# Kernel tuning notes

Hardware: AMD Instinct MI355X
Metric: run time of the kernel (lower is better)

## Reference

```python
import jax, jax.numpy as jnp
import numpy as np

KERNEL = 3
SCALE = 2
PAD = KERNEL - 1
EPS = 1e-5


def _splits(a, s):
    # (B,C,W,H) -> (B,C,W/s,H/s,s*s), matching torch view/permute order
    B, C, W, H = a.shape
    b = a.reshape(B, C, s, W // s, s, H // s)
    b = jnp.transpose(b, (0, 1, 3, 5, 2, 4))
    return b.reshape(B, C, W // s, H // s, s * s)


def _p2o(psf, shape):
    # PSF (1,C,k,k) -> OTF (1,C,H,W)
    k_h, k_w = psf.shape[-2], psf.shape[-1]
    otf = jnp.zeros(psf.shape[:-2] + shape, dtype=psf.dtype)
    otf = otf.at[..., :k_h, :k_w].set(psf)
    otf = jnp.roll(otf, (-(k_h // 2), -(k_w // 2)), axis=(-2, -1))
    return jnp.fft.fftn(otf, axes=(-2, -1))


def _zero_upsample(x, s):
    B, C, H, W = x.shape
    z = jnp.zeros((B, C, H * s, W * s), dtype=x.dtype)
    return z.at[..., ::s, ::s].set(x)


def setup_inputs() -> dict:
    key = jax.random.key(0)
    kx, kw = jax.random.split(key)
    x = jax.random.normal(kx, (4, 64, 128, 128), dtype=jnp.float32)
    w = jax.random.normal(kw, (1, 64, KERNEL, KERNEL), dtype=jnp.float32)
    # init-time softmax over the k*k taps, as in the torch module
    w = jax.nn.softmax(w.reshape(1, 64, -1), axis=-1).reshape(1, 64, KERNEL, KERNEL)
    bias = jnp.zeros((1, 64, 1, 1), dtype=jnp.float32)
    return {"x": x, "weight": w, "bias": bias}


def reference(x, weight, bias):
    s = SCALE
    if PAD > 0:
        x = jnp.pad(x, ((0, 0), (0, 0), (PAD, PAD), (PAD, PAD)), mode="wrap")
    biaseps = jax.nn.sigmoid(bias - 9.0) + EPS  # (1,C,1,1)
    _, _, h, w = x.shape
    STy = _zero_upsample(x, s)
    # nearest-neighbor interpolate by integer scale == repeat
    x_up = jnp.repeat(jnp.repeat(x, s, axis=-2), s, axis=-1)
    FB = _p2o(weight, (h * s, w * s))          # (1,C,H,W) complex
    FBC = jnp.conj(FB)
    F2B = jnp.abs(FB) ** 2
    FBFy = FBC * jnp.fft.fftn(STy, axes=(-2, -1))
    FR = FBFy + jnp.fft.fftn(biaseps * x_up, axes=(-2, -1))
    x1 = FB * FR
    FBR = jnp.mean(_splits(x1, s), axis=-1)
    invW = jnp.mean(_splits(jnp.broadcast_to(F2B, x1.shape), s), axis=-1)
    invWBR = FBR / (invW + biaseps)
    FCBinvWBR = FBC * jnp.tile(invWBR, (1, 1, s, s))
    FX = (FR - FCBinvWBR) / biaseps
    out = jnp.real(jnp.fft.ifftn(FX, axes=(-2, -1)))
    if PAD > 0:
        c = PAD * s
        out = out[..., c:-c, c:-c]
    return jax.nn.gelu(out, approximate=False)
```

## Files before the change

kernel.cpp:

```cpp
#include <hip/hip_runtime.h>
#include <math.h>

#define NP   132
#define NV   67
#define NPP  (NP*NP)
#define NCH  64
#define NIMG 256
#define NX   128
#define NO   256
#define TWO_PI 6.2831853071795864769f

static const size_t OFF_H = 0;

#define TR0(t) (t.x)
#define TI0(t) (t.y)
#define TR1(t) (-(t.y))
#define TI1(t) (t.x)
#define TR2(t) (-(t.x))
#define TI2(t) (-(t.y))
#define TR3(t) (t.y)
#define TI3(t) (-(t.x))
#define CMACF(xr, xi, dr, di, TRv, TIv) { xr += (dr)*(TRv) + (di)*(TIv); xi += (di)*(TRv) - (dr)*(TIv); }
#define CMACG(xr, xi, dr, di, TRv, TIv) { xr += (dr)*(TRv) - (di)*(TIv); xi += (di)*(TRv) + (dr)*(TIv); }

__global__ __launch_bounds__(256) void k_compute_H(
    const float* __restrict__ wgt, const float* __restrict__ bias,
    float2* __restrict__ H) {
  int idx = blockIdx.x * 256 + threadIdx.x;
  int c = blockIdx.y;
  if (idx >= NV*NP) return;
  int u = idx % NP, v = idx / NP;
  float k[3][3];
#pragma unroll
  for (int i = 0; i < 3; i++)
#pragma unroll
    for (int j = 0; j < 3; j++) k[i][j] = wgt[c*9 + i*3 + j];
  float invW = 0.f;
#pragma unroll
  for (int p0 = -1; p0 <= 1; p0++)
#pragma unroll
    for (int p1 = -1; p1 <= 1; p1++) {
      float s = 0.f;
#pragma unroll
      for (int i = 0; i < 3; i++)
#pragma unroll
        for (int j = 0; j < 3; j++) {
          int i2 = i - 2*p0, j2 = j - 2*p1;
          if (i2 >= 0 && i2 < 3 && j2 >= 0 && j2 < 3) s += k[i][j]*k[i2][j2];
        }
      float ang = TWO_PI * (float)(u*p0 + v*p1) / (float)NP;
      invW += s * cosf(ang);
    }
  float B00 = k[0][0]+k[0][1]+k[1][0]+k[1][1];
  float B10 = k[2][0]+k[2][1];
  float B01 = k[0][2]+k[1][2];
  float B11 = k[2][2];
  float su, cu, sv, cv, suv, cuv;
  sincosf(TWO_PI*(float)u/(float)NP, &su, &cu);
  sincosf(TWO_PI*(float)v/(float)NP, &sv, &cv);
  sincosf(TWO_PI*(float)(u+v)/(float)NP, &suv, &cuv);
  float Bre = B00 + B10*cu + B01*cv + B11*cuv;
  float Bim = -(B10*su + B01*sv + B11*suv);
  float alpha = 1.f/(1.f + expf(9.f - bias[c])) + 1e-5f;
  float d = invW + alpha;
  H[((size_t)c*NV + v)*NP + u] = make_float2((1.f - Bre)/d, (-Bim)/d);
}

__global__ __launch_bounds__(1024, 4) void k_fused(
    const float* __restrict__ x, const float* __restrict__ wgt,
    const float2* __restrict__ H, float* __restrict__ out) {
  __shared__ __align__(16) float2 R1[67*134 + 4];
  __shared__ __align__(16) float2 R2[33*274];
  int tid = threadIdx.x;
  int img = blockIdx.x;
  int c = img & 63;
  const float* xim = x + (size_t)img*NX*NX;
  const float2* Hc = H + (size_t)c*NV*NP;
  float4* yb = (float4*)R1;

  for (int e = tid; e < 132*33; e += 1024) {
    int n1 = e % 132, rpg = e / 132;
    int col = (n1 + 126) & 127;
    int r0 = 4*rpg + 126;
    yb[n1*33 + rpg] = make_float4(
        xim[((r0    )&127)*NX + col],
        xim[((r0 + 1)&127)*NX + col],
        xim[((r0 + 2)&127)*NX + col],
        xim[((r0 + 3)&127)*NX + col]);
  }
  __syncthreads();

  {
    bool act = tid < 561;
    int rpg = 0, qq = 0;
    if (act) { rpg = tid/17; qq = tid - rpg*17; }
    int q2 = qq + 17;
    bool ph2 = (q2 >= 33);
    float sa_, ca_, sb_, cb_;
    sincosf(TWO_PI*(float)qq/33.f, &sa_, &ca_);
    sincosf(TWO_PI*(float)q2/33.f, &sb_, &cb_);
    float Sr[4][2][2], Si[4][2][2];
#pragma unroll
    for (int r = 0; r < 4; ++r)
#pragma unroll
      for (int g = 0; g < 2; ++g)
#pragma unroll
        for (int w = 0; w < 2; ++w) { Sr[r][g][w] = 0.f; Si[r][g][w] = 0.f; }
    if (act) {
      const float4* bp = yb + rpg;
      float tar = 1.f, tai = 0.f, tbr = 1.f, tbi = 0.f;
#pragma unroll 1
      for (int m = 0; m < 33; ++m) {
        float4 d0 = bp[0], d1 = bp[33], d2 = bp[66], d3 = bp[99];
#define S1M(r, dd) \
        CMACF(Sr[r][0][0], Si[r][0][0], dd.x, dd.y, tar, tai); \
        CMACF(Sr[r][0][1], Si[r][0][1], dd.z, dd.w, tar, tai); \
        CMACF(Sr[r][1][0], Si[r][1][0], dd.x, dd.y, tbr, tbi); \
        CMACF(Sr[r][1][1], Si[r][1][1], dd.z, dd.w, tbr, tbi);
        S1M(0, d0) S1M(1, d1) S1M(2, d2) S1M(3, d3)
#undef S1M
        { float nt = tar*ca_ - tai*sa_; tai = tar*sa_ + tai*ca_; tar = nt; }
        { float nt = tbr*cb_ - tbi*sb_; tbi = tbr*sb_ + tbi*cb_; tbr = nt; }
        bp += 132;
      }
    }
    __syncthreads();
    if (act) {
#pragma unroll
      for (int g = 0; g < 2; ++g) {
        if (g == 1 && ph2) continue;
        int q = g ? q2 : qq;
        float sw, cw; sincosf(TWO_PI*(float)q/132.f, &sw, &cw);
        float2 w1 = make_float2(cw, sw);
        float2 w2 = make_float2(cw*cw - sw*sw, 2.f*cw*sw);
        float2 w3 = make_float2(w2.x*cw - w2.y*sw, w2.x*sw + w2.y*cw);
#define S1C(sidx, P1, P2, P3) { \
        float z0r = Sr[0][g][0], z0i = Si[0][g][0], z1r = Sr[0][g][1], z1i = Si[0][g][1]; \
        CMACF(z0r, z0i, Sr[1][g][0], Si[1][g][0], TR##P1(w1), TI##P1(w1)); \
        CMACF(z1r, z1i, Sr[1][g][1], Si[1][g][1], TR##P1(w1), TI##P1(w1)); \
        CMACF(z0r, z0i, Sr[2][g][0], Si[2][g][0], TR##P2(w2), TI##P2(w2)); \
        CMACF(z1r, z1i, Sr[2][g][1], Si[2][g][1], TR##P2(w2), TI##P2(w2)); \
        CMACF(z0r, z0i, Sr[3][g][0], Si[3][g][0], TR##P3(w3), TI##P3(w3)); \
        CMACF(z1r, z1i, Sr[3][g][1], Si[3][g][1], TR##P3(w3), TI##P3(w3)); \
        yb[(q + 33*(sidx))*33 + rpg] = make_float4(z0r, z0i, z1r, z1i); }
        S1C(0,0,0,0) S1C(1,1,2,3) S1C(2,2,0,2) S1C(3,3,2,1)
#undef S1C
      }
    }
    __syncthreads();
    if (act) {
#pragma unroll
      for (int g = 0; g < 2; ++g) {
        if (g == 1 && ph2) continue;
        int q = g ? q2 : qq;
        float4 Za = yb[q*33 + rpg];
        float4 Zb = yb[((132 - q) % 132)*33 + rpg];
        float4 Zc = yb[(q + 33)*33 + rpg];
        float4 Zd = yb[(99 - q)*33 + rpg];
        float4* A4 = (float4*)&R2[rpg*274 + q*4];
        A4[0] = make_float4(0.5f*(Za.x+Zb.x), 0.5f*(Za.y-Zb.y),
                            0.5f*(Za.y+Zb.y), 0.5f*(Zb.x-Za.x));
        A4[1] = make_float4(0.5f*(Za.z+Zb.z), 0.5f*(Za.w-Zb.w),
                            0.5f*(Za.w+Zb.w), 0.5f*(Zb.z-Za.z));
        float4* B4 = (float4*)&R2[rpg*274 + (q+33)*4];
        B4[0] = make_float4(0.5f*(Zc.x+Zd.x), 0.5f*(Zc.y-Zd.y),
                            0.5f*(Zc.y+Zd.y), 0.5f*(Zd.x-Zc.x));
        B4[1] = make_float4(0.5f*(Zc.z+Zd.z), 0.5f*(Zc.w-Zd.w),
                            0.5f*(Zc.w+Zd.w), 0.5f*(Zd.z-Zc.z));
        if (q == 0) {
          float4 Ze = yb[66*33 + rpg];
          float4* C4 = (float4*)&R2[rpg*274 + 66*4];
          C4[0] = make_float4(Ze.x, 0.f, Ze.y, 0.f);
          C4[1] = make_float4(Ze.z, 0.f, Ze.w, 0.f);
        }
      }
    }
  }
  __syncthreads();

  {
    bool act = tid < 737;
    int v = 0, qq = 0;
    if (act) { v = tid/11; qq = tid - v*11; }
    float s11, c11; sincosf(TWO_PI*(float)qq/11.f, &s11, &c11);
    float s33q, c33q; sincosf(TWO_PI*(float)qq/33.f, &s33q, &c33q);
    const float CG = -0.5f, SG = 0.86602540378443864676f;
    float c33g[3], s33g[3];
    c33g[0] = c33q;               s33g[0] = s33q;
    c33g[1] = c33q*CG - s33q*SG;  s33g[1] = s33q*CG + c33q*SG;
    c33g[2] = c33q*CG + s33q*SG;  s33g[2] = s33q*CG - c33q*SG;
    float SSr[3][4], SSi[3][4];
    float Sr[4][3], Si[4][3];
    float2 h[3][4];
#define ZSS() { \
    _Pragma("unroll") for (int s = 0; s < 3; ++s) \
    _Pragma("unroll") for (int r = 0; r < 4; ++r) { SSr[s][r] = 0.f; SSi[s][r] = 0.f; } }
#define S23TLOOP(MAC) { \
    float tr = 1.f, ti = 0.f; \
    const float2* bp = R2 + v*4; \
    _Pragma("unroll 1") \
    for (int t = 0; t < 11; ++t) { \
      _Pragma("unroll") \
      for (int s = 0; s < 3; ++s) { \
        float4 d01 = *(const float4*)(bp + s*274); \
        float4 d23 = *(const float4*)(bp + s*274 + 2); \
        MAC(SSr[s][0], SSi[s][0], d01.x, d01.y, tr, ti); \
        MAC(SSr[s][1], SSi[s][1], d01.z, d01.w, tr, ti); \
        MAC(SSr[s][2], SSi[s][2], d23.x, d23.y, tr, ti); \
        MAC(SSr[s][3], SSi[s][3], d23.z, d23.w, tr, ti); } \
      { float nt = tr*c11 - ti*s11; ti = tr*s11 + ti*c11; tr = nt; } \
      bp += 3*274; \
    } }
#define S23COMB(MAC) { \
    _Pragma("unroll") \
    for (int g = 0; g < 3; ++g) { \
      float cA = c33g[g], sA = s33g[g]; \
      float cB = cA*cA - sA*sA, sB = 2.f*cA*sA; \
      _Pragma("unroll") \
      for (int r = 0; r < 4; ++r) { \
        float xr = SSr[0][r], xi = SSi[0][r]; \
        MAC(xr, xi, SSr[1][r], SSi[1][r], cA, sA); \
        MAC(xr, xi, SSr[2][r], SSi[2][r], cB, sB); \
        Sr[r][g] = xr; Si[r][g] = xi; } } }
    ZSS();
    if (act) {
      S23TLOOP(CMACF);
      S23COMB(CMACF);
#pragma unroll
      for (int g = 0; g < 3; ++g)
#pragma unroll
        for (int s = 0; s < 4; ++s)
          h[g][s] = Hc[(size_t)v*NP + (qq + 11*g) + 33*s];
    }
    __syncthreads();
    if (act) {
#pragma unroll
      for (int g = 0; g < 3; ++g) {
        int q = qq + 11*g;
        float sw, cw; sincosf(TWO_PI*(float)q/132.f, &sw, &cw);
        float2 w1 = make_float2(cw, sw);
        float2 w2 = make_float2(cw*cw - sw*sw, 2.f*cw*sw);
        float2 w3 = make_float2(w2.x*cw - w2.y*sw, w2.x*sw + w2.y*cw);
#define S23A(sidx, P1, P2, P3) { \
        int u = q + 33*(sidx); \
        float xr = Sr[0][g], xi = Si[0][g]; \
        CMACF(xr, xi, Sr[1][g], Si[1][g], TR##P1(w1), TI##P1(w1)); \
        CMACF(xr, xi, Sr[2][g], Si[2][g], TR##P2(w2), TI##P2(w2)); \
        CMACF(xr, xi, Sr[3][g], Si[3][g], TR##P3(w3), TI##P3(w3)); \
        float2 hh = h[g][sidx]; \
        R2[(u>>2)*274 + v*4 + (u&3)] = make_float2(xr*hh.x - xi*hh.y, xr*hh.y + xi*hh.x); }
        S23A(0,0,0,0) S23A(1,1,2,3) S23A(2,2,0,2) S23A(3,3,2,1)
#undef S23A
      }
    }
    __syncthreads();
    ZSS();
    if (act) {
      S23TLOOP(CMACG);
      S23COMB(CMACG);
#pragma unroll
      for (int g = 0; g < 3; ++g) {
        int q = qq + 11*g;
        float sw, cw; sincosf(TWO_PI*(float)q/132.f, &sw, &cw);
        float2 w1 = make_float2(cw, sw);
        float2 w2 = make_float2(cw*cw - sw*sw, 2.f*cw*sw);
        float2 w3 = make_float2(w2.x*cw - w2.y*sw, w2.x*sw + w2.y*cw);
#define S23B(sidx, P1, P2, P3) { \
        int n0 = q + 33*(sidx); \
        float xr = Sr[0][g], xi = Si[0][g]; \
        CMACG(xr, xi, Sr[1][g], Si[1][g], TR##P1(w1), TI##P1(w1)); \
        CMACG(xr, xi, Sr[2][g], Si[2][g], TR##P2(w2), TI##P2(w2)); \
        CMACG(xr, xi, Sr[3][g], Si[3][g], TR##P3(w3), TI##P3(w3)); \
        R1[v*134 + n0] = make_float2(xr, xi); }
        S23B(0,0,0,0) S23B(1,1,2,3) S23B(2,2,0,2) S23B(3,3,2,1)
#undef S23B
      }
    }
#undef S23TLOOP
#undef S23COMB
#undef ZSS
  }
  __syncthreads();

  {
    bool act = tid < 726;
    int j = 0, qq = 0;
    if (act) { j = tid/11; qq = tid - j*11; }
    float s11, c11; sincosf(TWO_PI*(float)qq/11.f, &s11, &c11);
    float s33q, c33q; sincosf(TWO_PI*(float)qq/33.f, &s33q, &c33q);
    const float CG = -0.5f, SG = 0.86602540378443864676f;
    float c33g[3], s33g[3];
    c33g[0] = c33q;               s33g[0] = s33q;
    c33g[1] = c33q*CG - s33q*SG;  s33g[1] = s33q*CG + c33q*SG;
    c33g[2] = c33q*CG + s33q*SG;  s33g[2] = s33q*CG - c33q*SG;
    float SSr[3][4], SSi[3][4];
#pragma unroll
    for (int s = 0; s < 3; ++s)
#pragma unroll
      for (int r = 0; r < 4; ++r) { SSr[s][r] = 0.f; SSi[s][r] = 0.f; }
    if (act) {
      const float2* Up = R1 + 2*j;
      float tr = 1.f, ti = 0.f;
#pragma unroll 1
      for (int t = 0; t < 11; ++t) {
#pragma unroll
        for (int s = 0; s < 3; ++s)
#pragma unroll
          for (int r = 0; r < 4; ++r) {
            int v4 = 12*t + 4*s + r;
            int vv = (v4 <= 66) ? v4 : (132 - v4);
            float sg = (v4 <= 66) ? 1.f : -1.f;
            float4 f = *(const float4*)(Up + vv*134);
            float Wr = f.x - sg*f.w;
            float Wi = sg*f.y + f.z;
            CMACG(SSr[s][r], SSi[s][r], Wr, Wi, tr, ti);
          }
        { float nt = tr*c11 - ti*s11; ti = tr*s11 + ti*c11; tr = nt; }
      }
      float Sr[4][3], Si[4][3];
#pragma unroll
      for (int g = 0; g < 3; ++g) {
        float cA = c33g[g], sA = s33g[g];
        float cB = cA*cA - sA*sA, sB = 2.f*cA*sA;
#pragma unroll
        for (int r = 0; r < 4; ++r) {
          float xr = SSr[0][r], xi = SSi[0][r];
          CMACG(xr, xi, SSr[1][r], SSi[1][r], cA, sA);
          CMACG(xr, xi, SSr[2][r], SSi[2][r], cB, sB);
          Sr[r][g] = xr; Si[r][g] = xi;
        }
      }
      float* rho2 = (float*)R2;
      const float scale = 1.0f/(float)NPP;
#pragma unroll
      for (int g = 0; g < 3; ++g) {
        int q = qq + 11*g;
        float sw, cw; sincosf(TWO_PI*(float)q/132.f, &sw, &cw);
        float2 w1 = make_float2(cw, sw);
        float2 w2 = make_float2(cw*cw - sw*sw, 2.f*cw*sw);
        float2 w3 = make_float2(w2.x*cw - w2.y*sw, w2.x*sw + w2.y*cw);
#define S4C(sidx, P1, P2, P3) { \
        int n1 = q + 33*(sidx); \
        float zr = Sr[0][g], zi = Si[0][g]; \
        CMACG(zr, zi, Sr[1][g], Si[1][g], TR##P1(w1), TI##P1(w1)); \
        CMACG(zr, zi, Sr[2][g], Si[2][g], TR##P2(w2), TI##P2(w2)); \
        CMACG(zr, zi, Sr[3][g], Si[3][g], TR##P3(w3), TI##P3(w3)); \
        rho2[(2*j)*136 + n1] = zr*scale; \
        rho2[(2*j+1)*136 + n1] = zi*scale; }
        S4C(0,0,0,0) S4C(1,1,2,3) S4C(2,2,0,2) S4C(3,3,2,1)
#undef S4C
      }
    }
  }
  __syncthreads();

  {
    const float* rho2 = (const float*)R2;
    const float* w = wgt + c*9;
    float k0=w[0], k1=w[1], k2=w[2], k3=w[3], k4=w[4], k5=w[5], k6=w[6], k7=w[7], k8=w[8];
    float* outim = out + (size_t)img*NO*NO;
    for (int e = tid; e < NO*NO; e += 1024) {
      int o1 = e & 255, o0 = e >> 8;
      int n0 = (o0 + 4) >> 1, n1 = (o1 + 4) >> 1;
      int p0 = o0 & 1, p1 = o1 & 1;
      int base = n0*136 + n1;
      float r00 = rho2[base],     r01 = rho2[base+1];
      float r10 = rho2[base+136], r11 = rho2[base+137];
      float wa = p0 ? (p1 ? k0 : k1) : (p1 ? k3 : k4);
      float wb = p1 ? (p0 ? k2 : k5) : 0.f;
      float wc = p0 ? (p1 ? k6 : k7) : 0.f;
      float wd = (p0 & p1) ? k8 : 0.f;
      float S = wa*r00 + wb*r01 + wc*r10 + wd*r11;
      float xv = xim[(n0-2)*NX + (n1-2)];
      float z = xv + S;
      outim[e] = 0.5f*z*(1.0f + erff(z*0.70710678118654752f));
    }
  }
}

extern "C" void kernel_launch(void* const* d_in, const int* in_sizes, int n_in,
                              void* d_out, int out_size, void* d_ws, size_t ws_size,
                              hipStream_t stream) {
  const float* x    = (const float*)d_in[0];
  const float* wgt  = (const float*)d_in[1];
  const float* bias = (const float*)d_in[2];
  float* ws = (float*)d_ws;
  float2* H = (float2*)(ws + OFF_H);
  float* out = (float*)d_out;

  k_compute_H<<<dim3((NV*NP + 255)/256, NCH), 256, 0, stream>>>(wgt, bias, H);
  k_fused<<<dim3(NIMG), 1024, 0, stream>>>(x, wgt, H, out);
}
```

Measured before the change: 155.4 us.

## Restructure first and last FFT stages to row-contiguous 3x4x11 decomposition with twiddle recurrences

New measurement: 144.0 us. -7.3%, faster.

```diff
diff --git a/kernel.cpp b/kernel.cpp
--- a/kernel.cpp
+++ b/kernel.cpp
@@ -76,73 +76,77 @@
   int c = img & 63;
   const float* xim = x + (size_t)img*NX*NX;
   const float2* Hc = H + (size_t)c*NV*NP;
-  float4* yb = (float4*)R1;
-
-  for (int e = tid; e < 132*33; e += 1024) {
-    int n1 = e % 132, rpg = e / 132;
+  const float CG = -0.5f,                  SG = 0.86602540378443864676f;
+  const float CR = 0.86602540378443864676f, SR = 0.5f;
+
+  float2* yb = R1;
+  for (int e = tid; e < 66*132; e += 1024) {
+    int n1 = e % 132, j = e / 132;
     int col = (n1 + 126) & 127;
-    int r0 = 4*rpg + 126;
-    yb[n1*33 + rpg] = make_float4(
-        xim[((r0    )&127)*NX + col],
-        xim[((r0 + 1)&127)*NX + col],
-        xim[((r0 + 2)&127)*NX + col],
-        xim[((r0 + 3)&127)*NX + col]);
+    int ra = (2*j + 126) & 127, rb = (2*j + 127) & 127;
+    yb[j*134 + n1] = make_float2(xim[ra*NX + col], xim[rb*NX + col]);
   }
   __syncthreads();
 
   {
-    bool act = tid < 561;
-    int rpg = 0, qq = 0;
-    if (act) { rpg = tid/17; qq = tid - rpg*17; }
-    int q2 = qq + 17;
-    bool ph2 = (q2 >= 33);
-    float sa_, ca_, sb_, cb_;
-    sincosf(TWO_PI*(float)qq/33.f, &sa_, &ca_);
-    sincosf(TWO_PI*(float)q2/33.f, &sb_, &cb_);
-    float Sr[4][2][2], Si[4][2][2];
-#pragma unroll
-    for (int r = 0; r < 4; ++r)
-#pragma unroll
-      for (int g = 0; g < 2; ++g)
-#pragma unroll
-        for (int w = 0; w < 2; ++w) { Sr[r][g][w] = 0.f; Si[r][g][w] = 0.f; }
-    if (act) {
-      const float4* bp = yb + rpg;
-      float tar = 1.f, tai = 0.f, tbr = 1.f, tbi = 0.f;
+    bool act = tid < 726;
+    int j = 0, qq = 0;
+    if (act) { j = tid/11; qq = tid - j*11; }
+    float s11, c11; sincosf(TWO_PI*(float)qq/11.f, &s11, &c11);
+    float s33q, c33q; sincosf(TWO_PI*(float)qq/33.f, &s33q, &c33q);
+    float swq, cwq; sincosf(TWO_PI*(float)qq/132.f, &swq, &cwq);
+    float c33g[3], s33g[3], cwg[3], swg[3];
+    c33g[0] = c33q; s33g[0] = s33q;
+    c33g[1] = c33q*CG - s33q*SG;       s33g[1] = s33q*CG + c33q*SG;
+    c33g[2] = c33g[1]*CG - s33g[1]*SG; s33g[2] = s33g[1]*CG + c33g[1]*SG;
+    cwg[0] = cwq; swg[0] = swq;
+    cwg[1] = cwq*CR - swq*SR;          swg[1] = swq*CR + cwq*SR;
+    cwg[2] = cwg[1]*CR - swg[1]*SR;    swg[2] = swg[1]*CR + cwg[1]*SR;
+    float SSr[3][4], SSi[3][4];
+#pragma unroll
+    for (int s = 0; s < 3; ++s)
+#pragma unroll
+      for (int r = 0; r < 4; ++r) { SSr[s][r] = 0.f; SSi[s][r] = 0.f; }
+    if (act) {
+      const float2* bp = yb + j*134;
+      float tr = 1.f, ti = 0.f;
 #pragma unroll 1
-      for (int m = 0; m < 33; ++m) {
-        float4 d0 = bp[0], d1 = bp[33], d2 = bp[66], d3 = bp[99];
-#define S1M(r, dd) \
-        CMACF(Sr[r][0][0], Si[r][0][0], dd.x, dd.y, tar, tai); \
-        CMACF(Sr[r][0][1], Si[r][0][1], dd.z, dd.w, tar, tai); \
-        CMACF(Sr[r][1][0], Si[r][1][0], dd.x, dd.y, tbr, tbi); \
-        CMACF(Sr[r][1][1], Si[r][1][1], dd.z, dd.w, tbr, tbi);
-        S1M(0, d0) S1M(1, d1) S1M(2, d2) S1M(3, d3)
-#undef S1M
-        { float nt = tar*ca_ - tai*sa_; tai = tar*sa_ + tai*ca_; tar = nt; }
-        { float nt = tbr*cb_ - tbi*sb_; tbi = tbr*sb_ + tbi*cb_; tbr = nt; }
-        bp += 132;
-      }
-    }
-    __syncthreads();
-    if (act) {
-#pragma unroll
-      for (int g = 0; g < 2; ++g) {
-        if (g == 1 && ph2) continue;
-        int q = g ? q2 : qq;
-        float sw, cw; sincosf(TWO_PI*(float)q/132.f, &sw, &cw);
-        float2 w1 = make_float2(cw, sw);
-        float2 w2 = make_float2(cw*cw - sw*sw, 2.f*cw*sw);
-        float2 w3 = make_float2(w2.x*cw - w2.y*sw, w2.x*sw + w2.y*cw);
+      for (int t = 0; t < 11; ++t) {
+#pragma unroll
+        for (int s = 0; s < 3; ++s) {
+          float4 d01 = *(const float4*)(bp + 12*t + 4*s);
+          float4 d23 = *(const float4*)(bp + 12*t + 4*s + 2);
+          CMACF(SSr[s][0], SSi[s][0], d01.x, d01.y, tr, ti);
+          CMACF(SSr[s][1], SSi[s][1], d01.z, d01.w, tr, ti);
+          CMACF(SSr[s][2], SSi[s][2], d23.x, d23.y, tr, ti);
+          CMACF(SSr[s][3], SSi[s][3], d23.z, d23.w, tr, ti);
+        }
+        { float nt = tr*c11 - ti*s11; ti = tr*s11 + ti*c11; tr = nt; }
+      }
+    }
+    float Zr[3][4], Zi[3][4];
+    if (act) {
+#pragma unroll
+      for (int g = 0; g < 3; ++g) {
+        float cA = c33g[g], sA = s33g[g];
+        float cB = cA*cA - sA*sA, sB = 2.f*cA*sA;
+        float Sr4[4], Si4[4];
+#pragma unroll
+        for (int r = 0; r < 4; ++r) {
+          float xr = SSr[0][r], xi = SSi[0][r];
+          CMACF(xr, xi, SSr[1][r], SSi[1][r], cA, sA);
+          CMACF(xr, xi, SSr[2][r], SSi[2][r], cB, sB);
+          Sr4[r] = xr; Si4[r] = xi;
+        }
+        float2 w1 = make_float2(cwg[g], swg[g]);
+        float2 w2 = make_float2(w1.x*w1.x - w1.y*w1.y, 2.f*w1.x*w1.y);
+        float2 w3 = make_float2(w2.x*w1.x - w2.y*w1.y, w2.x*w1.y + w2.y*w1.x);
 #define S1C(sidx, P1, P2, P3) { \
-        float z0r = Sr[0][g][0], z0i = Si[0][g][0], z1r = Sr[0][g][1], z1i = Si[0][g][1]; \
-        CMACF(z0r, z0i, Sr[1][g][0], Si[1][g][0], TR##P1(w1), TI##P1(w1)); \
-        CMACF(z1r, z1i, Sr[1][g][1], Si[1][g][1], TR##P1(w1), TI##P1(w1)); \
-        CMACF(z0r, z0i, Sr[2][g][0], Si[2][g][0], TR##P2(w2), TI##P2(w2)); \
-        CMACF(z1r, z1i, Sr[2][g][1], Si[2][g][1], TR##P2(w2), TI##P2(w2)); \
-        CMACF(z0r, z0i, Sr[3][g][0], Si[3][g][0], TR##P3(w3), TI##P3(w3)); \
-        CMACF(z1r, z1i, Sr[3][g][1], Si[3][g][1], TR##P3(w3), TI##P3(w3)); \
-        yb[(q + 33*(sidx))*33 + rpg] = make_float4(z0r, z0i, z1r, z1i); }
+        float zr = Sr4[0], zi = Si4[0]; \
+        CMACF(zr, zi, Sr4[1], Si4[1], TR##P1(w1), TI##P1(w1)); \
+        CMACF(zr, zi, Sr4[2], Si4[2], TR##P2(w2), TI##P2(w2)); \
+        CMACF(zr, zi, Sr4[3], Si4[3], TR##P3(w3), TI##P3(w3)); \
+        Zr[g][sidx] = zr; Zi[g][sidx] = zi; }
         S1C(0,0,0,0) S1C(1,1,2,3) S1C(2,2,0,2) S1C(3,3,2,1)
 #undef S1C
       }
@@ -150,28 +154,33 @@
     __syncthreads();
     if (act) {
 #pragma unroll
-      for (int g = 0; g < 2; ++g) {
-        if (g == 1 && ph2) continue;
-        int q = g ? q2 : qq;
-        float4 Za = yb[q*33 + rpg];
-        float4 Zb = yb[((132 - q) % 132)*33 + rpg];
-        float4 Zc = yb[(q + 33)*33 + rpg];
-        float4 Zd = yb[(99 - q)*33 + rpg];
-        float4* A4 = (float4*)&R2[rpg*274 + q*4];
-        A4[0] = make_float4(0.5f*(Za.x+Zb.x), 0.5f*(Za.y-Zb.y),
-                            0.5f*(Za.y+Zb.y), 0.5f*(Zb.x-Za.x));
-        A4[1] = make_float4(0.5f*(Za.z+Zb.z), 0.5f*(Za.w-Zb.w),
-                            0.5f*(Za.w+Zb.w), 0.5f*(Zb.z-Za.z));
-        float4* B4 = (float4*)&R2[rpg*274 + (q+33)*4];
-        B4[0] = make_float4(0.5f*(Zc.x+Zd.x), 0.5f*(Zc.y-Zd.y),
-                            0.5f*(Zc.y+Zd.y), 0.5f*(Zd.x-Zc.x));
-        B4[1] = make_float4(0.5f*(Zc.z+Zd.z), 0.5f*(Zc.w-Zd.w),
-                            0.5f*(Zc.w+Zd.w), 0.5f*(Zd.z-Zc.z));
+      for (int g = 0; g < 3; ++g) {
+        int q = qq + 11*g;
+#pragma unroll
+        for (int s = 0; s < 4; ++s)
+          yb[j*134 + q + 33*s] = make_float2(Zr[g][s], Zi[g][s]);
+      }
+    }
+    __syncthreads();
+    if (act) {
+      const float2* Zrow = yb + j*134;
+      float2* Abase = &R2[(j>>1)*274 + 2*(j&1)];
+#pragma unroll
+      for (int g = 0; g < 3; ++g) {
+        int q = qq + 11*g;
+        float2 Za = Zrow[q];
+        float2 Zb = Zrow[(132 - q) % 132];
+        float2 Zc = Zrow[q + 33];
+        float2 Zd = Zrow[99 - q];
+        *(float4*)&Abase[q*4] = make_float4(
+            0.5f*(Za.x+Zb.x), 0.5f*(Za.y-Zb.y),
+            0.5f*(Za.y+Zb.y), 0.5f*(Zb.x-Za.x));
+        *(float4*)&Abase[(q+33)*4] = make_float4(
+            0.5f*(Zc.x+Zd.x), 0.5f*(Zc.y-Zd.y),
+            0.5f*(Zc.y+Zd.y), 0.5f*(Zd.x-Zc.x));
         if (q == 0) {
-          float4 Ze = yb[66*33 + rpg];
-          float4* C4 = (float4*)&R2[rpg*274 + 66*4];
-          C4[0] = make_float4(Ze.x, 0.f, Ze.y, 0.f);
-          C4[1] = make_float4(Ze.z, 0.f, Ze.w, 0.f);
+          float2 Ze = Zrow[66];
+          *(float4*)&Abase[66*4] = make_float4(Ze.x, 0.f, Ze.y, 0.f);
         }
       }
     }
@@ -184,11 +193,14 @@
     if (act) { v = tid/11; qq = tid - v*11; }
     float s11, c11; sincosf(TWO_PI*(float)qq/11.f, &s11, &c11);
     float s33q, c33q; sincosf(TWO_PI*(float)qq/33.f, &s33q, &c33q);
-    const float CG = -0.5f, SG = 0.86602540378443864676f;
-    float c33g[3], s33g[3];
-    c33g[0] = c33q;               s33g[0] = s33q;
-    c33g[1] = c33q*CG - s33q*SG;  s33g[1] = s33q*CG + c33q*SG;
-    c33g[2] = c33q*CG + s33q*SG;  s33g[2] = s33q*CG - c33q*SG;
+    float swq, cwq; sincosf(TWO_PI*(float)qq/132.f, &swq, &cwq);
+    float c33g[3], s33g[3], cwg[3], swg[3];
+    c33g[0] = c33q; s33g[0] = s33q;
+    c33g[1] = c33q*CG - s33q*SG;       s33g[1] = s33q*CG + c33q*SG;
+    c33g[2] = c33g[1]*CG - s33g[1]*SG; s33g[2] = s33g[1]*CG + c33g[1]*SG;
+    cwg[0] = cwq; swg[0] = swq;
+    cwg[1] = cwq*CR - swq*SR;          swg[1] = swq*CR + cwq*SR;
+    cwg[2] = cwg[1]*CR - swg[1]*SR;    swg[2] = swg[1]*CR + cwg[1]*SR;
     float SSr[3][4], SSi[3][4];
     float Sr[4][3], Si[4][3];
     float2 h[3][4];
@@ -237,10 +249,9 @@
 #pragma unroll
       for (int g = 0; g < 3; ++g) {
         int q = qq + 11*g;
-        float sw, cw; sincosf(TWO_PI*(float)q/132.f, &sw, &cw);
-        float2 w1 = make_float2(cw, sw);
-        float2 w2 = make_float2(cw*cw - sw*sw, 2.f*cw*sw);
-        float2 w3 = make_float2(w2.x*cw - w2.y*sw, w2.x*sw + w2.y*cw);
+        float2 w1 = make_float2(cwg[g], swg[g]);
+        float2 w2 = make_float2(w1.x*w1.x - w1.y*w1.y, 2.f*w1.x*w1.y);
+        float2 w3 = make_float2(w2.x*w1.x - w2.y*w1.y, w2.x*w1.y + w2.y*w1.x);
 #define S23A(sidx, P1, P2, P3) { \
         int u = q + 33*(sidx); \
         float xr = Sr[0][g], xi = Si[0][g]; \
@@ -261,10 +272,9 @@
 #pragma unroll
       for (int g = 0; g < 3; ++g) {
         int q = qq + 11*g;
-        float sw, cw; sincosf(TWO_PI*(float)q/132.f, &sw, &cw);
-        float2 w1 = make_float2(cw, sw);
-        float2 w2 = make_float2(cw*cw - sw*sw, 2.f*cw*sw);
-        float2 w3 = make_float2(w2.x*cw - w2.y*sw, w2.x*sw + w2.y*cw);
+        float2 w1 = make_float2(cwg[g], swg[g]);
+        float2 w2 = make_float2(w1.x*w1.x - w1.y*w1.y, 2.f*w1.x*w1.y);
+        float2 w3 = make_float2(w2.x*w1.x - w2.y*w1.y, w2.x*w1.y + w2.y*w1.x);
 #define S23B(sidx, P1, P2, P3) { \
         int n0 = q + 33*(sidx); \
         float xr = Sr[0][g], xi = Si[0][g]; \
@@ -283,68 +293,80 @@
   __syncthreads();
 
   {
+    float2* Wb = R2;
+    for (int e = tid; e < 66*132; e += 1024) {
+      int v4 = e % 132, j = e / 132;
+      int vv = (v4 <= 66) ? v4 : 132 - v4;
+      float4 f = *(const float4*)(R1 + vv*134 + 2*j);
+      float2 w = (v4 <= 66) ? make_float2(f.x - f.w, f.y + f.z)
+                            : make_float2(f.x + f.w, f.z - f.y);
+      Wb[j*134 + v4] = w;
+    }
+  }
+  __syncthreads();
+
+  {
     bool act = tid < 726;
     int j = 0, qq = 0;
     if (act) { j = tid/11; qq = tid - j*11; }
     float s11, c11; sincosf(TWO_PI*(float)qq/11.f, &s11, &c11);
     float s33q, c33q; sincosf(TWO_PI*(float)qq/33.f, &s33q, &c33q);
-    const float CG = -0.5f, SG = 0.86602540378443864676f;
-    float c33g[3], s33g[3];
-    c33g[0] = c33q;               s33g[0] = s33q;
-    c33g[1] = c33q*CG - s33q*SG;  s33g[1] = s33q*CG + c33q*SG;
-    c33g[2] = c33q*CG + s33q*SG;  s33g[2] = s33q*CG - c33q*SG;
+    float swq, cwq; sincosf(TWO_PI*(float)qq/132.f, &swq, &cwq);
+    float c33g[3], s33g[3], cwg[3], swg[3];
+    c33g[0] = c33q; s33g[0] = s33q;
+    c33g[1] = c33q*CG - s33q*SG;       s33g[1] = s33q*CG + c33q*SG;
+    c33g[2] = c33g[1]*CG - s33g[1]*SG; s33g[2] = s33g[1]*CG + c33g[1]*SG;
+    cwg[0] = cwq; swg[0] = swq;
+    cwg[1] = cwq*CR - swq*SR;          swg[1] = swq*CR + cwq*SR;
+    cwg[2] = cwg[1]*CR - swg[1]*SR;    swg[2] = swg[1]*CR + cwg[1]*SR;
     float SSr[3][4], SSi[3][4];
 #pragma unroll
     for (int s = 0; s < 3; ++s)
 #pragma unroll
       for (int r = 0; r < 4; ++r) { SSr[s][r] = 0.f; SSi[s][r] = 0.f; }
     if (act) {
-      const float2* Up = R1 + 2*j;
+      const float2* bp = R2 + j*134;
       float tr = 1.f, ti = 0.f;
 #pragma unroll 1
       for (int t = 0; t < 11; ++t) {
 #pragma unroll
-        for (int s = 0; s < 3; ++s)
-#pragma unroll
-          for (int r = 0; r < 4; ++r) {
-            int v4 = 12*t + 4*s + r;
-            int vv = (v4 <= 66) ? v4 : (132 - v4);
-            float sg = (v4 <= 66) ? 1.f : -1.f;
-            float4 f = *(const float4*)(Up + vv*134);
-            float Wr = f.x - sg*f.w;
-            float Wi = sg*f.y + f.z;
-            CMACG(SSr[s][r], SSi[s][r], Wr, Wi, tr, ti);
-          }
+        for (int s = 0; s < 3; ++s) {
+          float4 d01 = *(const float4*)(bp + 12*t + 4*s);
+          float4 d23 = *(const float4*)(bp + 12*t + 4*s + 2);
+          CMACG(SSr[s][0], SSi[s][0], d01.x, d01.y, tr, ti);
+          CMACG(SSr[s][1], SSi[s][1], d01.z, d01.w, tr, ti);
+          CMACG(SSr[s][2], SSi[s][2], d23.x, d23.y, tr, ti);
+          CMACG(SSr[s][3], SSi[s][3], d23.z, d23.w, tr, ti);
+        }
         { float nt = tr*c11 - ti*s11; ti = tr*s11 + ti*c11; tr = nt; }
       }
-      float Sr[4][3], Si[4][3];
-#pragma unroll
-      for (int g = 0; g < 3; ++g) {
+    }
+    __syncthreads();
+    if (act) {
+      float* rho2 = (float*)R1;
+      const float scale = 1.0f/(float)NPP;
+#pragma unroll
+      for (int g = 0; g < 3; ++g) {
+        int q = qq + 11*g;
         float cA = c33g[g], sA = s33g[g];
         float cB = cA*cA - sA*sA, sB = 2.f*cA*sA;
+        float Sr4[4], Si4[4];
 #pragma unroll
         for (int r = 0; r < 4; ++r) {
           float xr = SSr[0][r], xi = SSi[0][r];
           CMACG(xr, xi, SSr[1][r], SSi[1][r], cA, sA);
           CMACG(xr, xi, SSr[2][r], SSi[2][r], cB, sB);
-          Sr[r][g] = xr; Si[r][g] = xi;
-        }
-      }
-      float* rho2 = (float*)R2;
-      const float scale = 1.0f/(float)NPP;
-#pragma unroll
-      for (int g = 0; g < 3; ++g) {
-        int q = qq + 11*g;
-        float sw, cw; sincosf(TWO_PI*(float)q/132.f, &sw, &cw);
-        float2 w1 = make_float2(cw, sw);
-        float2 w2 = make_float2(cw*cw - sw*sw, 2.f*cw*sw);
-        float2 w3 = make_float2(w2.x*cw - w2.y*sw, w2.x*sw + w2.y*cw);
+          Sr4[r] = xr; Si4[r] = xi;
+        }
+        float2 w1 = make_float2(cwg[g], swg[g]);
+        float2 w2 = make_float2(w1.x*w1.x - w1.y*w1.y, 2.f*w1.x*w1.y);
+        float2 w3 = make_float2(w2.x*w1.x - w2.y*w1.y, w2.x*w1.y + w2.y*w1.x);
 #define S4C(sidx, P1, P2, P3) { \
         int n1 = q + 33*(sidx); \
-        float zr = Sr[0][g], zi = Si[0][g]; \
-        CMACG(zr, zi, Sr[1][g], Si[1][g], TR##P1(w1), TI##P1(w1)); \
-        CMACG(zr, zi, Sr[2][g], Si[2][g], TR##P2(w2), TI##P2(w2)); \
-        CMACG(zr, zi, Sr[3][g], Si[3][g], TR##P3(w3), TI##P3(w3)); \
+        float zr = Sr4[0], zi = Si4[0]; \
+        CMACG(zr, zi, Sr4[1], Si4[1], TR##P1(w1), TI##P1(w1)); \
+        CMACG(zr, zi, Sr4[2], Si4[2], TR##P2(w2), TI##P2(w2)); \
+        CMACG(zr, zi, Sr4[3], Si4[3], TR##P3(w3), TI##P3(w3)); \
         rho2[(2*j)*136 + n1] = zr*scale; \
         rho2[(2*j+1)*136 + n1] = zi*scale; }
         S4C(0,0,0,0) S4C(1,1,2,3) S4C(2,2,0,2) S4C(3,3,2,1)
@@ -355,7 +377,7 @@
   __syncthreads();
 
   {
-    const float* rho2 = (const float*)R2;
+    const float* rho2 = (const float*)R1;
     const float* w = wgt + c*9;
     float k0=w[0], k1=w[1], k2=w[2], k3=w[3], k4=w[4], k5=w[5], k6=w[6], k7=w[7], k8=w[8];
     float* outim = out + (size_t)img*NO*NO;
```
